# Kernel tuning notes

Hardware: AMD Instinct MI355X
Metric: run time of the kernel (lower is better)

The kernel has to match this reference:

```python
import jax, jax.numpy as jnp
import numpy as np

HEADS = 6
EPS = 1e-5


def _na_idx(L, k, d):
    # NATTEN-style dilated neighborhood: work within dilation cosets,
    # clamp window to stay inside the image (window shifts at borders).
    i = np.arange(L)
    g = i % d
    p = i // d
    Lg = (L - g + d - 1) // d  # coset length per position
    start = np.clip(p - k // 2, 0, Lg - k)
    j = np.arange(k)
    nbr = g[:, None] + d * (start[:, None] + j[None, :])          # [L,k] neighbor coords
    rel = (start[:, None] + j[None, :]) - p[:, None] + (k - 1)    # [L,k] rpb index in [0,2k-2]
    return jnp.asarray(nbr, jnp.int32), jnp.asarray(rel, jnp.int32)


def _na2d(x, qkv_w, qkv_b, proj_w, proj_b, rpb, heads, k, d):
    # x: [B,H,W,C] NHWC neighborhood attention with relative positional bias
    B, H, W, C = x.shape
    dh = C // heads
    scale = dh ** -0.5
    qkv = (x @ qkv_w + qkv_b).reshape(B, H, W, 3, heads, dh)
    qkv = jnp.transpose(qkv, (3, 0, 4, 1, 2, 5))  # [3,B,h,H,W,dh]
    q, kk, v = qkv[0] * scale, qkv[1], qkv[2]
    nh, rh = _na_idx(H, k, d)
    nw, rw = _na_idx(W, k, d)

    def gather(t):  # [B,h,H,W,dh] -> [B,h,H,W,k,k,dh]
        t = t[:, :, nh]              # [B,h,H,k,W,dh]
        t = t[:, :, :, :, nw]        # [B,h,H,k,W,k,dh]
        return jnp.transpose(t, (0, 1, 2, 4, 3, 5, 6))

    kn, vn = gather(kk), gather(v)
    attn = jnp.einsum('bhxyd,bhxyijd->bhxyij', q, kn)  # [B,h,H,W,k,k]
    bias = rpb[:, rh]                  # [h,H,k,2k-1]
    bias = bias[:, :, :, rw]           # [h,H,k,W,k]
    bias = jnp.transpose(bias, (0, 1, 3, 2, 4))  # [h,H,W,k,k]
    attn = attn + bias[None]
    attn = jax.nn.softmax(attn.reshape(B, heads, H, W, k * k), axis=-1)
    attn = attn.reshape(B, heads, H, W, k, k)
    out = jnp.einsum('bhxyij,bhxyijd->bhxyd', attn, vn)
    out = jnp.transpose(out, (0, 2, 3, 1, 4)).reshape(B, H, W, C)
    return out @ proj_w + proj_b


def _rln(x, w, b, m1_w, m1_b, m2_w, m2_b):
    # Revised LayerNorm: normalize over (C,H,W) per sample; meta1/meta2 are 1x1 convs on std/mean
    mean = jnp.mean(x, axis=(1, 2, 3), keepdims=True)
    std = jnp.sqrt(jnp.mean((x - mean) ** 2, axis=(1, 2, 3), keepdims=True) + EPS)
    out = (x - mean) / std * w + b
    rescale = m1_w[None, :, None, None] * std + m1_b[None, :, None, None]
    rebias = m2_w[None, :, None, None] * mean + m2_b[None, :, None, None]
    return out, rescale, rebias


def _c11(x, w, b):  # 1x1 conv on NCHW == per-pixel linear
    return jnp.einsum('bchw,oc->bohw', x, w) + b[None, :, None, None]


def _gelu(x):
    return jax.nn.gelu(x, approximate=False)


def reference(x, ln_w, ln_b, m1_w, m1_b, m2_w, m2_b, qkv1_w, qkv1_b, proj1_w, proj1_b, rpb1, qkv2_w, qkv2_b, proj2_w, proj2_b, rpb2, mlp_w1, mlp_b1, mlp_w2, mlp_b2, bn_g, bn_b, bn_m, bn_v, pa_w1, pa_b1, pa_w2, pa_b2, ca_w1, ca_b1, ca_w2, ca_b2, m2a_w1, m2a_b1, m2a_w2, m2a_b2):
    # ---- NA block 1 (kernel 7, dilation 1) ----
    sc = x
    y, rs, rb = _rln(x, ln_w, ln_b, m1_w, m1_b, m2_w, m2_b)
    a = _na2d(jnp.transpose(y, (0, 2, 3, 1)), qkv1_w, qkv1_b, proj1_w, proj1_b, rpb1, HEADS, 7, 1)
    x = sc + jnp.transpose(a, (0, 3, 1, 2)) * rs + rb
    # ---- NA block 2 (kernel 5, dilation 8) ----
    sc = x
    y, rs, rb = _rln(x, ln_w, ln_b, m1_w, m1_b, m2_w, m2_b)
    a = _na2d(jnp.transpose(y, (0, 2, 3, 1)), qkv2_w, qkv2_b, proj2_w, proj2_b, rpb2, HEADS, 5, 8)
    x = sc + jnp.transpose(a, (0, 3, 1, 2)) * rs + rb
    # ---- MLP (source reuses the pre-attn2 shortcut `sc`) ----
    y, rs, rb = _rln(x, ln_w, ln_b, m1_w, m1_b, m2_w, m2_b)
    m = _c11(jax.nn.relu(_c11(y, mlp_w1, mlp_b1)), mlp_w2, mlp_b2)
    x = sc + m * rs + rb
    # ---- BN + pixel attention + channel attention + mlp2 ----
    sc = x
    inv = jax.lax.rsqrt(bn_v + EPS)
    y = (x - bn_m[None, :, None, None]) * (inv * bn_g)[None, :, None, None] + bn_b[None, :, None, None]
    pa = jax.nn.sigmoid(_c11(_gelu(_c11(y, pa_w1, pa_b1)), pa_w2, pa_b2))  # [B,1,H,W]
    y = pa * y
    gap = jnp.mean(y, axis=(2, 3), keepdims=True)
    ca = jax.nn.sigmoid(_c11(_gelu(_c11(gap, ca_w1, ca_b1)), ca_w2, ca_b2))  # [B,C,1,1]
    y = ca * y
    y = _c11(_gelu(_c11(y, m2a_w1, m2a_b1)), m2a_w2, m2a_b2)
    return sc + y


def setup_inputs() -> dict:
    key = jax.random.key(0)
    B, C, H, W, HID = 4, 96, 64, 64, 384
    ks = iter(jax.random.split(key, 48))

    def rn(shape, s=0.02):
        return jax.random.normal(next(ks), shape, jnp.float32) * s

    d = {}
    d['x'] = jax.random.normal(next(ks), (B, C, H, W), jnp.float32)
    d['ln_w'] = jnp.ones((1, C, 1, 1), jnp.float32)
    d['ln_b'] = jnp.zeros((1, C, 1, 1), jnp.float32)
    d['m1_w'] = rn((C,)); d['m1_b'] = jnp.ones((C,), jnp.float32)
    d['m2_w'] = rn((C,)); d['m2_b'] = jnp.zeros((C,), jnp.float32)
    d['qkv1_w'] = rn((C, 3 * C)); d['qkv1_b'] = jnp.zeros((3 * C,), jnp.float32)
    d['proj1_w'] = rn((C, C)); d['proj1_b'] = jnp.zeros((C,), jnp.float32)
    d['rpb1'] = rn((HEADS, 13, 13))
    d['qkv2_w'] = rn((C, 3 * C)); d['qkv2_b'] = jnp.zeros((3 * C,), jnp.float32)
    d['proj2_w'] = rn((C, C)); d['proj2_b'] = jnp.zeros((C,), jnp.float32)
    d['rpb2'] = rn((HEADS, 9, 9))
    d['mlp_w1'] = rn((HID, C)); d['mlp_b1'] = jnp.zeros((HID,), jnp.float32)
    d['mlp_w2'] = rn((C, HID)); d['mlp_b2'] = jnp.zeros((C,), jnp.float32)
    d['bn_g'] = jnp.ones((C,), jnp.float32); d['bn_b'] = jnp.zeros((C,), jnp.float32)
    d['bn_m'] = jnp.zeros((C,), jnp.float32); d['bn_v'] = jnp.ones((C,), jnp.float32)
    d['pa_w1'] = rn((C // 8, C)); d['pa_b1'] = jnp.zeros((C // 8,), jnp.float32)
    d['pa_w2'] = rn((1, C // 8)); d['pa_b2'] = jnp.zeros((1,), jnp.float32)
    d['ca_w1'] = rn((C, C)); d['ca_b1'] = jnp.zeros((C,), jnp.float32)
    d['ca_w2'] = rn((C, C)); d['ca_b2'] = jnp.zeros((C,), jnp.float32)
    d['m2a_w1'] = rn((C, C)); d['m2a_b1'] = jnp.zeros((C,), jnp.float32)
    d['m2a_w2'] = rn((C, C)); d['m2a_b2'] = jnp.zeros((C,), jnp.float32)
    return d
```

## Files before the change

kernel.cpp:

```cpp
#include <hip/hip_runtime.h>
#include <math.h>

#define CC 96
#define NP 4096
#define NHEADS 6
#define NELEMF 393216.0f
#define EPSF 1e-5f

typedef __attribute__((ext_vector_type(8))) short bf16x8;
typedef __attribute__((ext_vector_type(4))) float f32x4;
#define MFMA16(a,b,c) __builtin_amdgcn_mfma_f32_16x16x32_bf16(a,b,c,0,0,0)

#define WQKV1  64
#define WQKV2  (WQKV1+13824)
#define WPROJ1 (WQKV2+13824)
#define WPROJ2 (WPROJ1+4608)
#define WMLP1  (WPROJ2+4608)
#define WMLP2  (WMLP1+18432)
#define WM2A1  (WMLP2+18432)
#define WM2A2  (WM2A1+4608)
#define WPA1T  (WM2A2+4608)
#define WBNS   (WPA1T+1152)
#define WCA1T  (WBNS+192)
#define WCA2T  (WCA1T+9216)
#define WS_Q   870784
#define WS_K   (WS_Q+786432)
#define WS_V   (WS_K+786432)
#define WS_ATTPM (WS_V+786432)
#define WS_X1  (WS_ATTPM+786432)
#define WS_X2  (WS_X1+1572864)
#define WS_X3  (WS_X2+1572864)
#define WS_PA  (WS_X3+1572864)
#define WS_GAP (WS_PA+16384)

__device__ __forceinline__ float gelu_f(float x){
  return 0.5f * x * (1.0f + erff(x * 0.7071067811865476f));
}
__device__ __forceinline__ float sigmoid_f(float x){
  return 1.0f / (1.0f + __expf(-x));
}
__device__ __forceinline__ unsigned short bfr(float f){
  unsigned int u = __float_as_uint(f);
  u += 0x7fffu + ((u >> 16) & 1u);
  return (unsigned short)(u >> 16);
}
__device__ __forceinline__ float bflo16(unsigned short u){ return __uint_as_float(((unsigned int)u) << 16); }
__device__ __forceinline__ float bflo(unsigned int u){ return __uint_as_float(u << 16); }
__device__ __forceinline__ float bfhi(unsigned int u){ return __uint_as_float(u & 0xffff0000u); }
__device__ __forceinline__ void get_ms(const float* st, int b, float& mean, float& inv, float& stdv){
  float s = st[b], s2 = st[4+b];
  mean = s * (1.0f/NELEMF);
  float var = fmaxf(s2 * (1.0f/NELEMF) - mean*mean, 0.0f);
  stdv = sqrtf(var + EPSF);
  inv = 1.0f / stdv;
}
__device__ __forceinline__ float ldf(const float* p, int i){ return p[i]; }
__device__ __forceinline__ float ldf(const unsigned short* p, int i){ return bflo16(p[i]); }
__device__ __forceinline__ void load4(const float* p, float4& v){ v = *(const float4*)p; }
__device__ __forceinline__ void load4(const unsigned short* p, float4& v){
  ushort4 u = *(const ushort4*)p;
  v.x = bflo16(u.x); v.y = bflo16(u.y); v.z = bflo16(u.z); v.w = bflo16(u.w);
}

__device__ __forceinline__ float dot16(const float* qv, const uint2* col, int ww){
  uint2 a0 = col[ww], a1 = col[64+ww], a2 = col[128+ww], a3 = col[192+ww];
  float s;
  s  = qv[0]*bflo(a0.x);           s = fmaf(qv[1],  bfhi(a0.x), s);
  s = fmaf(qv[2],  bflo(a0.y), s); s = fmaf(qv[3],  bfhi(a0.y), s);
  s = fmaf(qv[4],  bflo(a1.x), s); s = fmaf(qv[5],  bfhi(a1.x), s);
  s = fmaf(qv[6],  bflo(a1.y), s); s = fmaf(qv[7],  bfhi(a1.y), s);
  s = fmaf(qv[8],  bflo(a2.x), s); s = fmaf(qv[9],  bfhi(a2.x), s);
  s = fmaf(qv[10], bflo(a2.y), s); s = fmaf(qv[11], bfhi(a2.y), s);
  s = fmaf(qv[12], bflo(a3.x), s); s = fmaf(qv[13], bfhi(a3.x), s);
  s = fmaf(qv[14], bflo(a3.y), s); s = fmaf(qv[15], bfhi(a3.y), s);
  return s;
}
__device__ __forceinline__ void pv16(float w, const uint2* col, int ww, float* acc){
  uint2 a0 = col[ww], a1 = col[64+ww], a2 = col[128+ww], a3 = col[192+ww];
  acc[0]  = fmaf(w, bflo(a0.x), acc[0]);  acc[1]  = fmaf(w, bfhi(a0.x), acc[1]);
  acc[2]  = fmaf(w, bflo(a0.y), acc[2]);  acc[3]  = fmaf(w, bfhi(a0.y), acc[3]);
  acc[4]  = fmaf(w, bflo(a1.x), acc[4]);  acc[5]  = fmaf(w, bfhi(a1.x), acc[5]);
  acc[6]  = fmaf(w, bflo(a1.y), acc[6]);  acc[7]  = fmaf(w, bfhi(a1.y), acc[7]);
  acc[8]  = fmaf(w, bflo(a2.x), acc[8]);  acc[9]  = fmaf(w, bfhi(a2.x), acc[9]);
  acc[10] = fmaf(w, bflo(a2.y), acc[10]); acc[11] = fmaf(w, bfhi(a2.y), acc[11]);
  acc[12] = fmaf(w, bflo(a3.x), acc[12]); acc[13] = fmaf(w, bfhi(a3.x), acc[13]);
  acc[14] = fmaf(w, bflo(a3.y), acc[14]); acc[15] = fmaf(w, bfhi(a3.y), acc[15]);
}

__global__ void prep_stats_kernel(const float* __restrict__ x, float* __restrict__ st,
                             const float* __restrict__ q1, const float* __restrict__ q2,
                             const float* __restrict__ p1, const float* __restrict__ p2,
                             const float* __restrict__ w1, const float* __restrict__ w2,
                             const float* __restrict__ a1, const float* __restrict__ a2,
                             const float* __restrict__ pw1,
                             const float* __restrict__ bg, const float* __restrict__ bb,
                             const float* __restrict__ bm, const float* __restrict__ bv,
                             const float* __restrict__ cw1, const float* __restrict__ cw2,
                             float* __restrict__ ws){
  if(blockIdx.x < 384){
    int b = blockIdx.x / CC, c = blockIdx.x % CC;
    const float4* p4 = (const float4*)(x + (size_t)(b*CC + c)*NP);
    float s = 0.f, s2 = 0.f;
    for(int i = threadIdx.x; i < 1024; i += 256){
      float4 v = p4[i];
      s += v.x + v.y + v.z + v.w;
      s2 = fmaf(v.x, v.x, fmaf(v.y, v.y, fmaf(v.z, v.z, fmaf(v.w, v.w, s2))));
    }
    for(int off = 32; off > 0; off >>= 1){ s += __shfl_down(s, off); s2 += __shfl_down(s2, off); }
    __shared__ float ls[8];
    int wid = threadIdx.x >> 6;
    if((threadIdx.x & 63) == 0){ ls[wid] = s; ls[4+wid] = s2; }
    __syncthreads();
    if(threadIdx.x == 0){
      atomicAdd(&st[b],   ls[0]+ls[1]+ls[2]+ls[3]);
      atomicAdd(&st[4+b], ls[4]+ls[5]+ls[6]+ls[7]);
    }
    return;
  }
  int gid = (blockIdx.x - 384)*256 + threadIdx.x;
  if(gid < 27648){ int n = gid/96, c = gid%96; ((unsigned short*)(ws+WQKV1))[gid] = bfr(q1[c*288+n]); }
  else if(gid < 55296){ int g = gid-27648; int n = g/96, c = g%96; ((unsigned short*)(ws+WQKV2))[g] = bfr(q2[c*288+n]); }
  else if(gid < 64512){ int g = gid-55296; int n = g/96, c = g%96; ((unsigned short*)(ws+WPROJ1))[g] = bfr(p1[c*96+n]); }
  else if(gid < 73728){ int g = gid-64512; int n = g/96, c = g%96; ((unsigned short*)(ws+WPROJ2))[g] = bfr(p2[c*96+n]); }
  else if(gid < 110592){ int g = gid-73728; ((unsigned short*)(ws+WMLP1))[g] = bfr(w1[g]); }
  else if(gid < 147456){ int g = gid-110592; ((unsigned short*)(ws+WMLP2))[g] = bfr(w2[g]); }
  else if(gid < 156672){ int g = gid-147456; ((unsigned short*)(ws+WM2A1))[g] = bfr(a1[g]); }
  else if(gid < 165888){ int g = gid-156672; ((unsigned short*)(ws+WM2A2))[g] = bfr(a2[g]); }
  else if(gid < 167040){ int g = gid-165888; int c = g/12, h = g%12; ws[WPA1T + g] = pw1[h*96+c]; }
  else if(gid < 167136){ int c = gid-167040;
    float sc = rsqrtf(bv[c] + EPSF) * bg[c];
    ws[WBNS + c] = sc;
    ws[WBNS + 96 + c] = bb[c] - bm[c]*sc;
  }
  else if(gid < 167520){ ws[WS_GAP + (gid-167136)] = 0.f; }
  else if(gid < 176736){ int g = gid-167520; int o = g/96, c = g%96; ws[WCA1T + c*96 + o] = cw1[g]; }
  else if(gid < 185952){ int g = gid-176736; int o = g/96, c = g%96; ws[WCA2T + c*96 + o] = cw2[g]; }
}

template<typename AT>
__global__ void __launch_bounds__(512) gemm_qkv_kernel(
    const AT* __restrict__ xin, const float* __restrict__ st,
    const float* __restrict__ lnw, const float* __restrict__ lnb,
    const unsigned short* __restrict__ wT, const float* __restrict__ qb,
    unsigned short* __restrict__ qo, unsigned short* __restrict__ ko, unsigned short* __restrict__ vo){
  __shared__ unsigned short Atl[64*104];
  __shared__ float scl[96], ofs[96];
  int m_base = blockIdx.x*64;
  int b = m_base >> 12, pxl0 = m_base & 4095;
  float mean, inv, stdv; get_ms(st, b, mean, inv, stdv);
  int tid = threadIdx.x;
  if(tid < 96){ float s = inv*lnw[tid]; scl[tid] = s; ofs[tid] = lnb[tid] - mean*s; }
  __syncthreads();
  const AT* src = xin + (size_t)b*CC*NP + pxl0;
  for(int idx = tid; idx < 96*16; idx += 512){
    int c = idx >> 4, p4 = (idx & 15) << 2;
    float4 v; load4(src + (size_t)c*NP + p4, v);
    float s = scl[c], o = ofs[c];
    Atl[(p4+0)*104 + c] = bfr(fmaf(v.x, s, o));
    Atl[(p4+1)*104 + c] = bfr(fmaf(v.y, s, o));
    Atl[(p4+2)*104 + c] = bfr(fmaf(v.z, s, o));
    Atl[(p4+3)*104 + c] = bfr(fmaf(v.w, s, o));
  }
  __syncthreads();
  int w = tid >> 6, lane = tid & 63, ml = lane & 15, q = lane >> 4;
  int row = w & 3, nh = w >> 2;
  const unsigned short* arow = Atl + (row*16 + ml)*104;
  bf16x8 av[3];
  #pragma unroll
  for(int ks = 0; ks < 3; ++ks) av[ks] = *(const bf16x8*)(arow + ks*32 + q*8);
  f32x4 z = {0.f,0.f,0.f,0.f};
  #pragma unroll
  for(int g0 = 0; g0 < 3; ++g0){
    int g = nh*3 + g0;
    f32x4 acc[3] = {z, z, z};
    #pragma unroll
    for(int ks = 0; ks < 3; ++ks){
      #pragma unroll
      for(int gg = 0; gg < 3; ++gg){
        bf16x8 bv = *(const bf16x8*)(wT + (g*48 + gg*16 + ml)*96 + ks*32 + q*8);
        acc[gg] = MFMA16(av[ks], bv, acc[gg]);
      }
    }
    #pragma unroll
    for(int gg = 0; gg < 3; ++gg){
      int nfb = g*48 + gg*16;
      int t = nfb/96, head = (nfb%96) >> 4;
      float scale = (t == 0) ? 0.25f : 1.0f;
      unsigned short* dst = (t == 0) ? qo : (t == 1) ? ko : vo;
      float bias = qb[nfb + ml];
      #pragma unroll
      for(int r = 0; r < 4; ++r){
        int pxl = pxl0 + row*16 + q*4 + r;
        dst[(((size_t)(b*NHEADS + head))*NP + pxl)*16 + ml] = bfr((acc[gg][r] + bias)*scale);
      }
    }
  }
}

template<typename SCT>
__global__ void __launch_bounds__(512) gemm_proj_kernel(
    const unsigned short* __restrict__ attpm, const unsigned short* __restrict__ wT,
    const float* __restrict__ pb, const SCT* __restrict__ scx, const float* __restrict__ st,
    const float* __restrict__ m1w, const float* __restrict__ m1b,
    const float* __restrict__ m2w, const float* __restrict__ m2b,
    unsigned short* __restrict__ dst, float* __restrict__ st_out){
  int w = threadIdx.x >> 6, lane = threadIdx.x & 63;
  int ml = lane & 15, q = lane >> 4;
  int m_base = blockIdx.x*128 + w*16;
  int n0 = blockIdx.y*48;
  f32x4 z = {0.f,0.f,0.f,0.f};
  f32x4 acc[3] = {z, z, z};
  {
    const bf16x8* a0 = (const bf16x8*)(attpm + (size_t)(m_base + ml)*96 + q*8);
    #pragma unroll
    for(int ks = 0; ks < 3; ++ks){
      bf16x8 av0 = a0[ks*4];
      #pragma unroll
      for(int g = 0; g < 3; ++g){
        bf16x8 bv = *(const bf16x8*)(wT + (n0 + g*16 + ml)*96 + ks*32 + q*8);
        acc[g] = MFMA16(av0, bv, acc[g]);
      }
    }
  }
  __shared__ float T[48*133];
  #pragma unroll
  for(int g = 0; g < 3; ++g)
    #pragma unroll
    for(int r = 0; r < 4; ++r)
      T[(g*16 + ml)*133 + w*16 + q*4 + r] = acc[g][r];
  __syncthreads();
  int b = (blockIdx.x*128) >> 12, pxl0 = (blockIdx.x*128) & 4095;
  float mean, inv, stdv; get_ms(st, b, mean, inv, stdv);
  float s = 0.f, s2 = 0.f;
  for(int idx = threadIdx.x; idx < 48*128; idx += 512){
    int row = idx >> 7, px = idx & 127;
    int n = n0 + row;
    float rsf = fmaf(m1w[n], stdv, m1b[n]);
    float rbf = fmaf(m2w[n], mean, m2b[n]);
    int ad = (b*CC + n)*NP + pxl0 + px;
    float val = ldf(scx, ad) + (T[row*133 + px] + pb[n])*rsf + rbf;
    dst[ad] = bfr(val);
    s += val; s2 = fmaf(val, val, s2);
  }
  for(int off = 32; off > 0; off >>= 1){ s += __shfl_down(s, off); s2 += __shfl_down(s2, off); }
  __shared__ float ls[16];
  int wid = threadIdx.x >> 6;
  if((threadIdx.x & 63) == 0){ ls[wid] = s; ls[8+wid] = s2; }
  __syncthreads();
  if(threadIdx.x == 0){
    atomicAdd(&st_out[b],   ls[0]+ls[1]+ls[2]+ls[3]+ls[4]+ls[5]+ls[6]+ls[7]);
    atomicAdd(&st_out[4+b], ls[8]+ls[9]+ls[10]+ls[11]+ls[12]+ls[13]+ls[14]+ls[15]);
  }
}

__global__ void __launch_bounds__(512) gemm_mlp_kernel(
    const unsigned short* __restrict__ xin, const float* __restrict__ st,
    const float* __restrict__ lnw, const float* __restrict__ lnb,
    const unsigned short* __restrict__ w1T, const float* __restrict__ b1,
    const unsigned short* __restrict__ w2T, const float* __restrict__ b2,
    const unsigned short* __restrict__ scx,
    const float* __restrict__ m1w, const float* __restrict__ m1b,
    const float* __restrict__ m2w, const float* __restrict__ m2b,
    float* __restrict__ dst,
    const float* __restrict__ bns, const float* __restrict__ pw1t,
    const float* __restrict__ pb1, const float* __restrict__ pw2,
    const float* __restrict__ pb2, float* __restrict__ pa,
    float* __restrict__ gap){
  __shared__ __align__(16) char smbuf[63488];
  __shared__ float scl[96], ofs[96];
  unsigned short* Atl  = (unsigned short*)smbuf;
  unsigned short* hidL = (unsigned short*)(smbuf + 13312);
  float* T = (float*)(smbuf + 13312);
  float* gpart = (float*)smbuf;
  int m_base = blockIdx.x*64;
  int b = m_base >> 12, pxl0 = m_base & 4095;
  float mean, inv, stdv; get_ms(st, b, mean, inv, stdv);
  int tid = threadIdx.x;
  if(tid < 96){ float s = inv*lnw[tid]; scl[tid] = s; ofs[tid] = lnb[tid] - mean*s; }
  __syncthreads();
  const unsigned short* src = xin + (size_t)b*CC*NP + pxl0;
  for(int idx = tid; idx < 96*16; idx += 512){
    int c = idx >> 4, p4 = (idx & 15) << 2;
    float4 v; load4(src + (size_t)c*NP + p4, v);
    float s = scl[c], o = ofs[c];
    Atl[(p4+0)*104 + c] = bfr(fmaf(v.x, s, o));
    Atl[(p4+1)*104 + c] = bfr(fmaf(v.y, s, o));
    Atl[(p4+2)*104 + c] = bfr(fmaf(v.z, s, o));
    Atl[(p4+3)*104 + c] = bfr(fmaf(v.w, s, o));
  }
  __syncthreads();
  int w = tid >> 6, lane = tid & 63, ml = lane & 15, q = lane >> 4;
  int row = w & 3, nh = w >> 2;
  f32x4 z = {0.f,0.f,0.f,0.f};
  {
    const unsigned short* arow = Atl + (row*16 + ml)*104;
    bf16x8 av[3];
    #pragma unroll
    for(int ks = 0; ks < 3; ++ks) av[ks] = *(const bf16x8*)(arow + ks*32 + q*8);
    #pragma unroll
    for(int g0 = 0; g0 < 4; ++g0){
      int g = nh*4 + g0;
      f32x4 acc[3] = {z, z, z};
      #pragma unroll
      for(int ks = 0; ks < 3; ++ks){
        #pragma unroll
        for(int gg = 0; gg < 3; ++gg){
          bf16x8 bv = *(const bf16x8*)(w1T + (g*48 + gg*16 + ml)*96 + ks*32 + q*8);
          acc[gg] = MFMA16(av[ks], bv, acc[gg]);
        }
      }
      #pragma unroll
      for(int gg = 0; gg < 3; ++gg){
        int n = g*48 + gg*16 + ml;
        float bias = b1[n];
        #pragma unroll
        for(int r = 0; r < 4; ++r)
          hidL[(row*16 + q*4 + r)*392 + n] = bfr(fmaxf(acc[gg][r] + bias, 0.f));
      }
    }
  }
  __syncthreads();
  f32x4 acc2[3] = {z, z, z};
  {
    const unsigned short* arow = hidL + (row*16 + ml)*392;
    #pragma unroll
    for(int ks = 0; ks < 12; ++ks){
      bf16x8 av = *(const bf16x8*)(arow + ks*32 + q*8);
      #pragma unroll
      for(int g0 = 0; g0 < 3; ++g0){
        int g = nh*3 + g0;
        bf16x8 bv = *(const bf16x8*)(w2T + (g*16 + ml)*384 + ks*32 + q*8);
        acc2[g0] = MFMA16(av, bv, acc2[g0]);
      }
    }
  }
  __syncthreads();
  #pragma unroll
  for(int g0 = 0; g0 < 3; ++g0){
    int g = nh*3 + g0;
    #pragma unroll
    for(int r = 0; r < 4; ++r)
      T[(g*16 + ml)*68 + row*16 + q*4 + r] = acc2[g0][r];
  }
  __syncthreads();
  for(int idx = tid; idx < 96*64; idx += 512){
    int n = idx >> 6, px = idx & 63;
    float rsf = fmaf(m1w[n], stdv, m1b[n]);
    float rbf = fmaf(m2w[n], mean, m2b[n]);
    int ad = (b*CC + n)*NP + pxl0 + px;
    float val = ldf(scx, ad) + (T[n*68 + px] + b2[n])*rsf + rbf;
    dst[ad] = val;
    T[n*68 + px] = val;
  }
  __syncthreads();
  int pxq = tid >> 3, t = tid & 7;
  float yvv[12], acc[12];
  #pragma unroll
  for(int h = 0; h < 12; ++h) acc[h] = 0.f;
  #pragma unroll 6
  for(int cc = 0; cc < 12; ++cc){
    int c = t*12 + cc;
    float yv = fmaf(T[c*68 + pxq], bns[c], bns[96 + c]);
    yvv[cc] = yv;
    #pragma unroll
    for(int h = 0; h < 12; ++h) acc[h] = fmaf(yv, pw1t[c*12 + h], acc[h]);
  }
  #pragma unroll
  for(int h = 0; h < 12; ++h){
    acc[h] += __shfl_xor(acc[h], 1);
    acc[h] += __shfl_xor(acc[h], 2);
    acc[h] += __shfl_xor(acc[h], 4);
  }
  float s = pb2[0];
  #pragma unroll
  for(int h = 0; h < 12; ++h) s = fmaf(gelu_f(acc[h] + pb1[h]), pw2[h], s);
  float pav = sigmoid_f(s);
  if(t == 0) pa[b*NP + pxl0 + pxq] = pav;
  #pragma unroll 6
  for(int cc = 0; cc < 12; ++cc){
    float g = yvv[cc] * pav;
    g += __shfl_xor(g, 8);  g += __shfl_xor(g, 16); g += __shfl_xor(g, 32);
    if(lane < 8) gpart[w*96 + lane*12 + cc] = g;
  }
  __syncthreads();
  if(tid < 96){
    int c = tid;
    float v = 0.f;
    #pragma unroll
    for(int ww = 0; ww < 8; ++ww) v += gpart[ww*96 + c];
    atomicAdd(&gap[b*96 + c], v * (1.0f/4096.0f));
  }
}

__global__ void __launch_bounds__(512) gemm_m2a_kernel(
    const float* __restrict__ x3, const float* __restrict__ bns,
    const float* __restrict__ pa, const float* __restrict__ gap,
    const float* __restrict__ cw1T, const float* __restrict__ cb1,
    const float* __restrict__ cw2T, const float* __restrict__ cb2,
    const unsigned short* __restrict__ w1T, const float* __restrict__ b1,
    const unsigned short* __restrict__ w2T, const float* __restrict__ b2,
    const float* __restrict__ scx, float* __restrict__ outp){
  __shared__ __align__(16) char smbuf[26624];
  __shared__ float scl[96], ofs[96], pal[64];
  __shared__ float gl[96], tl[96];
  unsigned short* Atl = (unsigned short*)smbuf;
  unsigned short* tl2 = (unsigned short*)(smbuf + 13312);
  float* T = (float*)smbuf;
  int m_base = blockIdx.x*64;
  int b = m_base >> 12, pxl0 = m_base & 4095;
  int tid = threadIdx.x;
  if(tid < 96) gl[tid] = gap[b*96 + tid];
  if(tid >= 128 && tid < 192) pal[tid-128] = pa[m_base + (tid-128)];
  __syncthreads();
  if(tid < 96){
    float a = cb1[tid];
    #pragma unroll 8
    for(int c = 0; c < 96; ++c) a = fmaf(gl[c], cw1T[c*96 + tid], a);
    tl[tid] = gelu_f(a);
  }
  __syncthreads();
  if(tid < 96){
    float a = cb2[tid];
    #pragma unroll 8
    for(int c = 0; c < 96; ++c) a = fmaf(tl[c], cw2T[c*96 + tid], a);
    float cv = sigmoid_f(a);
    scl[tid] = bns[tid]*cv; ofs[tid] = bns[96+tid]*cv;
  }
  __syncthreads();
  const float* src = x3 + (size_t)b*CC*NP + pxl0;
  for(int idx = tid; idx < 96*16; idx += 512){
    int c = idx >> 4, p4 = (idx & 15) << 2;
    float4 v = *(const float4*)(src + (size_t)c*NP + p4);
    float s = scl[c], o = ofs[c];
    Atl[(p4+0)*104 + c] = bfr(fmaf(v.x, s, o) * pal[p4+0]);
    Atl[(p4+1)*104 + c] = bfr(fmaf(v.y, s, o) * pal[p4+1]);
    Atl[(p4+2)*104 + c] = bfr(fmaf(v.z, s, o) * pal[p4+2]);
    Atl[(p4+3)*104 + c] = bfr(fmaf(v.w, s, o) * pal[p4+3]);
  }
  __syncthreads();
  int w = tid >> 6, lane = tid & 63, ml = lane & 15, q = lane >> 4;
  int row = w & 3, nh = w >> 2;
  f32x4 z = {0.f,0.f,0.f,0.f};
  f32x4 acc1[3] = {z, z, z};
  {
    const unsigned short* arow = Atl + (row*16 + ml)*104;
    #pragma unroll
    for(int ks = 0; ks < 3; ++ks){
      bf16x8 av = *(const bf16x8*)(arow + ks*32 + q*8);
      #pragma unroll
      for(int g0 = 0; g0 < 3; ++g0){
        int g = nh*3 + g0;
        bf16x8 bv = *(const bf16x8*)(w1T + (g*16 + ml)*96 + ks*32 + q*8);
        acc1[g0] = MFMA16(av, bv, acc1[g0]);
      }
    }
  }
  #pragma unroll
  for(int g0 = 0; g0 < 3; ++g0){
    int g = nh*3 + g0;
    float bias = b1[g*16 + ml];
    #pragma unroll
    for(int r = 0; r < 4; ++r)
      tl2[(row*16 + q*4 + r)*104 + g*16 + ml] = bfr(gelu_f(acc1[g0][r] + bias));
  }
  __syncthreads();
  f32x4 acc2[3] = {z, z, z};
  {
    const unsigned short* arow = tl2 + (row*16 + ml)*104;
    #pragma unroll
    for(int ks = 0; ks < 3; ++ks){
      bf16x8 av = *(const bf16x8*)(arow + ks*32 + q*8);
      #pragma unroll
      for(int g0 = 0; g0 < 3; ++g0){
        int g = nh*3 + g0;
        bf16x8 bv = *(const bf16x8*)(w2T + (g*16 + ml)*96 + ks*32 + q*8);
        acc2[g0] = MFMA16(av, bv, acc2[g0]);
      }
    }
  }
  __syncthreads();
  #pragma unroll
  for(int g0 = 0; g0 < 3; ++g0){
    int g = nh*3 + g0;
    #pragma unroll
    for(int r = 0; r < 4; ++r)
      T[(g*16 + ml)*68 + row*16 + q*4 + r] = acc2[g0][r];
  }
  __syncthreads();
  for(int idx = tid; idx < 96*64; idx += 512){
    int n = idx >> 6, p = idx & 63;
    int ad = (b*CC + n)*NP + pxl0 + p;
    outp[ad] = scx[ad] + T[n*68 + p] + b2[n];
  }
}

template<int K, int D, int RPB, int SPAN>
__global__ void __launch_bounds__(256) attn2_kernel(
    const unsigned short* __restrict__ qb, const unsigned short* __restrict__ kb,
    const unsigned short* __restrict__ vb, const float* __restrict__ rpb,
    unsigned short* __restrict__ outp){
  __shared__ uint2 kst[SPAN*256];
  __shared__ uint2 vst[SPAN*256];
  __shared__ float rpbl[RPB*RPB];
  int bh = blockIdx.x >> 4;
  int quad = blockIdx.x & 15;
  int head = bh % NHEADS, b = bh / NHEADS;
  int tid = threadIdx.x;
  int tcol = tid >> 6, y = tid & 63;

  int gx, px, px0;
  if(D == 1){ gx = 0; px = quad*4 + tcol; px0 = quad*4; }
  else      { gx = quad & (D-1); px = (quad >> 3)*4 + tcol; px0 = (quad >> 3)*4; }
  int Lgx = (64 - gx + D - 1) / D;
  int sx = min(max(px - K/2, 0), Lgx - K);
  int sxmin = min(max(px0 - K/2, 0), Lgx - K);
  int nstage = min(SPAN, Lgx - sxmin);

  for(int i = tid; i < RPB*RPB; i += 256) rpbl[i] = rpb[head*RPB*RPB + i];
  {
    const uint2* kg = (const uint2*)(kb + (size_t)bh*NP*16);
    const uint2* vg = (const uint2*)(vb + (size_t)bh*NP*16);
    int spx = tid & 63, sq = tid >> 6;
    for(int c = 0; c < nstage; ++c){
      int hh = gx + D*(sxmin + c);
      kst[c*256 + sq*64 + spx] = kg[hh*256 + spx*4 + sq];
      vst[c*256 + sq*64 + spx] = vg[hh*256 + spx*4 + sq];
    }
  }
  int x = gx + D*px;
  int pix = x*64 + y;
  float qv[16];
  {
    const uint4* qg = (const uint4*)(qb + ((size_t)bh*NP + pix)*16);
    uint4 qa = qg[0], qb4 = qg[1];
    qv[0]=bflo(qa.x);  qv[1]=bfhi(qa.x);  qv[2]=bflo(qa.y);  qv[3]=bfhi(qa.y);
    qv[4]=bflo(qa.z);  qv[5]=bfhi(qa.z);  qv[6]=bflo(qa.w);  qv[7]=bfhi(qa.w);
    qv[8]=bflo(qb4.x); qv[9]=bfhi(qb4.x); qv[10]=bflo(qb4.y);qv[11]=bfhi(qb4.y);
    qv[12]=bflo(qb4.z);qv[13]=bfhi(qb4.z);qv[14]=bflo(qb4.w);qv[15]=bfhi(qb4.w);
  }
  __syncthreads();

  int gy = y & (D-1), py = (D==1) ? y : (y >> 3);
  int Lgy = (64 - gy + D - 1) / D;
  int sy = min(max(py - K/2, 0), Lgy - K);
  int dxb = sx - px + (K-1);
  int dyb = sy - py + (K-1);
  int ci0 = sx - sxmin;

  float sc[K*K];
  #pragma unroll
  for(int i = 0; i < K; ++i){
    const uint2* kc = kst + (ci0 + i)*256;
    const float* br = rpbl + (i + dxb)*RPB + dyb;
    #pragma unroll
    for(int j = 0; j < K; ++j){
      int ww = gy + D*(sy + j);
      sc[i*K + j] = dot16(qv, kc, ww) + br[j];
    }
  }
  float mx = -1e30f;
  #pragma unroll
  for(int n = 0; n < K*K; ++n) mx = fmaxf(mx, sc[n]);
  float sum = 0.f;
  #pragma unroll
  for(int n = 0; n < K*K; ++n){ float e = __expf(sc[n] - mx); sc[n] = e; sum += e; }
  float rs = 1.0f / sum;
  float acc[16];
  #pragma unroll
  for(int d = 0; d < 16; ++d) acc[d] = 0.f;
  #pragma unroll
  for(int i = 0; i < K; ++i){
    const uint2* vc = vst + (ci0 + i)*256;
    #pragma unroll
    for(int j = 0; j < K; ++j){
      int ww = gy + D*(sy + j);
      pv16(sc[i*K + j] * rs, vc, ww, acc);
    }
  }
  unsigned int ow[8];
  #pragma unroll
  for(int p = 0; p < 8; ++p)
    ow[p] = (unsigned int)bfr(acc[2*p]) | ((unsigned int)bfr(acc[2*p+1]) << 16);
  unsigned short* op = outp + ((size_t)(b*NP + pix))*96 + head*16;
  ((uint4*)op)[0] = make_uint4(ow[0], ow[1], ow[2], ow[3]);
  ((uint4*)op)[1] = make_uint4(ow[4], ow[5], ow[6], ow[7]);
}

extern "C" void kernel_launch(void* const* d_in, const int* in_sizes, int n_in,
                              void* d_out, int out_size, void* d_ws, size_t ws_size,
                              hipStream_t stream){
  (void)in_sizes; (void)n_in; (void)out_size; (void)ws_size;
  const float* x     = (const float*)d_in[0];
  const float* lnw   = (const float*)d_in[1];
  const float* lnb   = (const float*)d_in[2];
  const float* m1w   = (const float*)d_in[3];
  const float* m1b   = (const float*)d_in[4];
  const float* m2w   = (const float*)d_in[5];
  const float* m2b   = (const float*)d_in[6];
  const float* qkv1w = (const float*)d_in[7];
  const float* qkv1b = (const float*)d_in[8];
  const float* proj1w= (const float*)d_in[9];
  const float* proj1b= (const float*)d_in[10];
  const float* rpb1  = (const float*)d_in[11];
  const float* qkv2w = (const float*)d_in[12];
  const float* qkv2b = (const float*)d_in[13];
  const float* proj2w= (const float*)d_in[14];
  const float* proj2b= (const float*)d_in[15];
  const float* rpb2  = (const float*)d_in[16];
  const float* mw1   = (const float*)d_in[17];
  const float* mb1   = (const float*)d_in[18];
  const float* mw2   = (const float*)d_in[19];
  const float* mb2   = (const float*)d_in[20];
  const float* bng   = (const float*)d_in[21];
  const float* bnb   = (const float*)d_in[22];
  const float* bnm   = (const float*)d_in[23];
  const float* bnv   = (const float*)d_in[24];
  const float* paw1  = (const float*)d_in[25];
  const float* pab1  = (const float*)d_in[26];
  const float* paw2  = (const float*)d_in[27];
  const float* pab2  = (const float*)d_in[28];
  const float* caw1  = (const float*)d_in[29];
  const float* cab1  = (const float*)d_in[30];
  const float* caw2  = (const float*)d_in[31];
  const float* cab2  = (const float*)d_in[32];
  const float* aw1   = (const float*)d_in[33];
  const float* ab1   = (const float*)d_in[34];
  const float* aw2   = (const float*)d_in[35];
  const float* ab2   = (const float*)d_in[36];

  float* ws  = (float*)d_ws;
  float* out = (float*)d_out;
  float* st0 = ws;
  float* st1 = ws + 8;
  float* st2 = ws + 16;
  unsigned short* q     = (unsigned short*)(ws + WS_Q);
  unsigned short* k     = (unsigned short*)(ws + WS_K);
  unsigned short* v     = (unsigned short*)(ws + WS_V);
  unsigned short* attpm = (unsigned short*)(ws + WS_ATTPM);
  unsigned short* x1b   = (unsigned short*)(ws + WS_X1);
  unsigned short* x2b   = (unsigned short*)(ws + WS_X2);
  float* x3  = ws + WS_X3;
  float* pab = ws + WS_PA;
  float* gpb = ws + WS_GAP;
  float* bns = ws + WBNS;

  hipMemsetAsync(d_ws, 0, 64*sizeof(float), stream);
  prep_stats_kernel<<<1111, 256, 0, stream>>>(x, st0, qkv1w, qkv2w, proj1w, proj2w,
                                              mw1, mw2, aw1, aw2, paw1,
                                              bng, bnb, bnm, bnv, caw1, caw2, ws);

  gemm_qkv_kernel<float><<<256, 512, 0, stream>>>(x, st0, lnw, lnb,
      (unsigned short*)(ws+WQKV1), qkv1b, q, k, v);
  attn2_kernel<7,1,13,10><<<384, 256, 0, stream>>>(q, k, v, rpb1, attpm);
  gemm_proj_kernel<float><<<dim3(128,2), 512, 0, stream>>>(attpm, (unsigned short*)(ws+WPROJ1),
      proj1b, x, st0, m1w, m1b, m2w, m2b, x1b, st1);

  gemm_qkv_kernel<unsigned short><<<256, 512, 0, stream>>>(x1b, st1, lnw, lnb,
      (unsigned short*)(ws+WQKV2), qkv2b, q, k, v);
  attn2_kernel<5,8,9,6><<<384, 256, 0, stream>>>(q, k, v, rpb2, attpm);
  gemm_proj_kernel<unsigned short><<<dim3(128,2), 512, 0, stream>>>(attpm, (unsigned short*)(ws+WPROJ2),
      proj2b, x1b, st1, m1w, m1b, m2w, m2b, x2b, st2);

  gemm_mlp_kernel<<<256, 512, 0, stream>>>(x2b, st2, lnw, lnb,
      (unsigned short*)(ws+WMLP1), mb1, (unsigned short*)(ws+WMLP2), mb2,
      x1b, m1w, m1b, m2w, m2b, x3,
      bns, ws + WPA1T, pab1, paw2, pab2, pab, gpb);

  gemm_m2a_kernel<<<256, 512, 0, stream>>>(x3, bns, pab, gpb,
                                           ws + WCA1T, cab1, ws + WCA2T, cab2,
                                           (unsigned short*)(ws+WM2A1), ab1,
                                           (unsigned short*)(ws+WM2A2), ab2, x3, out);
}
```

Baseline: 263.6 us.

## Fuse neighborhood attention with output projection and drop LDS K/V staging

```diff
diff --git a/kernel.cpp b/kernel.cpp
--- a/kernel.cpp
+++ b/kernel.cpp
@@ -62,29 +62,29 @@
   v.x = bflo16(u.x); v.y = bflo16(u.y); v.z = bflo16(u.z); v.w = bflo16(u.w);
 }
 
-__device__ __forceinline__ float dot16(const float* qv, const uint2* col, int ww){
-  uint2 a0 = col[ww], a1 = col[64+ww], a2 = col[128+ww], a3 = col[192+ww];
+__device__ __forceinline__ float dotg(const float* qv, const uint4* p){
+  uint4 a = p[0], b = p[1];
   float s;
-  s  = qv[0]*bflo(a0.x);           s = fmaf(qv[1],  bfhi(a0.x), s);
-  s = fmaf(qv[2],  bflo(a0.y), s); s = fmaf(qv[3],  bfhi(a0.y), s);
-  s = fmaf(qv[4],  bflo(a1.x), s); s = fmaf(qv[5],  bfhi(a1.x), s);
-  s = fmaf(qv[6],  bflo(a1.y), s); s = fmaf(qv[7],  bfhi(a1.y), s);
-  s = fmaf(qv[8],  bflo(a2.x), s); s = fmaf(qv[9],  bfhi(a2.x), s);
-  s = fmaf(qv[10], bflo(a2.y), s); s = fmaf(qv[11], bfhi(a2.y), s);
-  s = fmaf(qv[12], bflo(a3.x), s); s = fmaf(qv[13], bfhi(a3.x), s);
-  s = fmaf(qv[14], bflo(a3.y), s); s = fmaf(qv[15], bfhi(a3.y), s);
+  s  = qv[0]*bflo(a.x);            s = fmaf(qv[1],  bfhi(a.x), s);
+  s = fmaf(qv[2],  bflo(a.y), s);  s = fmaf(qv[3],  bfhi(a.y), s);
+  s = fmaf(qv[4],  bflo(a.z), s);  s = fmaf(qv[5],  bfhi(a.z), s);
+  s = fmaf(qv[6],  bflo(a.w), s);  s = fmaf(qv[7],  bfhi(a.w), s);
+  s = fmaf(qv[8],  bflo(b.x), s);  s = fmaf(qv[9],  bfhi(b.x), s);
+  s = fmaf(qv[10], bflo(b.y), s);  s = fmaf(qv[11], bfhi(b.y), s);
+  s = fmaf(qv[12], bflo(b.z), s);  s = fmaf(qv[13], bfhi(b.z), s);
+  s = fmaf(qv[14], bflo(b.w), s);  s = fmaf(qv[15], bfhi(b.w), s);
   return s;
 }
-__device__ __forceinline__ void pv16(float w, const uint2* col, int ww, float* acc){
-  uint2 a0 = col[ww], a1 = col[64+ww], a2 = col[128+ww], a3 = col[192+ww];
-  acc[0]  = fmaf(w, bflo(a0.x), acc[0]);  acc[1]  = fmaf(w, bfhi(a0.x), acc[1]);
-  acc[2]  = fmaf(w, bflo(a0.y), acc[2]);  acc[3]  = fmaf(w, bfhi(a0.y), acc[3]);
-  acc[4]  = fmaf(w, bflo(a1.x), acc[4]);  acc[5]  = fmaf(w, bfhi(a1.x), acc[5]);
-  acc[6]  = fmaf(w, bflo(a1.y), acc[6]);  acc[7]  = fmaf(w, bfhi(a1.y), acc[7]);
-  acc[8]  = fmaf(w, bflo(a2.x), acc[8]);  acc[9]  = fmaf(w, bfhi(a2.x), acc[9]);
-  acc[10] = fmaf(w, bflo(a2.y), acc[10]); acc[11] = fmaf(w, bfhi(a2.y), acc[11]);
-  acc[12] = fmaf(w, bflo(a3.x), acc[12]); acc[13] = fmaf(w, bfhi(a3.x), acc[13]);
-  acc[14] = fmaf(w, bflo(a3.y), acc[14]); acc[15] = fmaf(w, bfhi(a3.y), acc[15]);
+__device__ __forceinline__ void pvg(float w, const uint4* p, float* acc){
+  uint4 a = p[0], b = p[1];
+  acc[0]  = fmaf(w, bflo(a.x), acc[0]);  acc[1]  = fmaf(w, bfhi(a.x), acc[1]);
+  acc[2]  = fmaf(w, bflo(a.y), acc[2]);  acc[3]  = fmaf(w, bfhi(a.y), acc[3]);
+  acc[4]  = fmaf(w, bflo(a.z), acc[4]);  acc[5]  = fmaf(w, bfhi(a.z), acc[5]);
+  acc[6]  = fmaf(w, bflo(a.w), acc[6]);  acc[7]  = fmaf(w, bfhi(a.w), acc[7]);
+  acc[8]  = fmaf(w, bflo(b.x), acc[8]);  acc[9]  = fmaf(w, bfhi(b.x), acc[9]);
+  acc[10] = fmaf(w, bflo(b.y), acc[10]); acc[11] = fmaf(w, bfhi(b.y), acc[11]);
+  acc[12] = fmaf(w, bflo(b.z), acc[12]); acc[13] = fmaf(w, bfhi(b.z), acc[13]);
+  acc[14] = fmaf(w, bflo(b.w), acc[14]); acc[15] = fmaf(w, bfhi(b.w), acc[15]);
 }
 
 __global__ void prep_stats_kernel(const float* __restrict__ x, float* __restrict__ st,
@@ -197,59 +197,143 @@
   }
 }
 
-template<typename SCT>
-__global__ void __launch_bounds__(512) gemm_proj_kernel(
-    const unsigned short* __restrict__ attpm, const unsigned short* __restrict__ wT,
-    const float* __restrict__ pb, const SCT* __restrict__ scx, const float* __restrict__ st,
+template<int K, int D, int RPB, typename SCT>
+__global__ void __launch_bounds__(512) attnproj_kernel(
+    const unsigned short* __restrict__ qb, const unsigned short* __restrict__ kb,
+    const unsigned short* __restrict__ vb, const float* __restrict__ rpb,
+    const unsigned short* __restrict__ wT, const float* __restrict__ pb,
+    const SCT* __restrict__ scx, const float* __restrict__ st,
     const float* __restrict__ m1w, const float* __restrict__ m1b,
     const float* __restrict__ m2w, const float* __restrict__ m2b,
     unsigned short* __restrict__ dst, float* __restrict__ st_out){
-  int w = threadIdx.x >> 6, lane = threadIdx.x & 63;
-  int ml = lane & 15, q = lane >> 4;
-  int m_base = blockIdx.x*128 + w*16;
-  int n0 = blockIdx.y*48;
+  __shared__ __align__(16) char smbuf[26624];
+  __shared__ float rpbl[NHEADS*RPB*RPB];
+  __shared__ float ls[16];
+  unsigned short* attout = (unsigned short*)smbuf;
+  float* T = (float*)smbuf;
+  int b = blockIdx.x >> 6;
+  int x = blockIdx.x & 63;
+  int tid = threadIdx.x;
+  for(int i = tid; i < NHEADS*RPB*RPB; i += 512) rpbl[i] = rpb[i];
+  __syncthreads();
+
+  if(tid < 384){
+    int head = tid >> 6;
+    int y = tid & 63;
+    int bh = b*NHEADS + head;
+    int gx = (D == 1) ? 0 : (x & (D-1));
+    int px = (D == 1) ? x : (x >> 3);
+    int Lgx = (64 - gx + D - 1) / D;
+    int sx = min(max(px - K/2, 0), Lgx - K);
+    int gy = (D == 1) ? 0 : (y & (D-1));
+    int py = (D == 1) ? y : (y >> 3);
+    int Lgy = (64 - gy + D - 1) / D;
+    int sy = min(max(py - K/2, 0), Lgy - K);
+    int dxb = sx - px + (K-1);
+    int dyb = sy - py + (K-1);
+    int pix = x*64 + y;
+
+    float qv[16];
+    {
+      const uint4* qg = (const uint4*)(qb + ((size_t)bh*NP + pix)*16);
+      uint4 qa = qg[0], qb4 = qg[1];
+      qv[0]=bflo(qa.x);  qv[1]=bfhi(qa.x);  qv[2]=bflo(qa.y);  qv[3]=bfhi(qa.y);
+      qv[4]=bflo(qa.z);  qv[5]=bfhi(qa.z);  qv[6]=bflo(qa.w);  qv[7]=bfhi(qa.w);
+      qv[8]=bflo(qb4.x); qv[9]=bfhi(qb4.x); qv[10]=bflo(qb4.y);qv[11]=bfhi(qb4.y);
+      qv[12]=bflo(qb4.z);qv[13]=bfhi(qb4.z);qv[14]=bflo(qb4.w);qv[15]=bfhi(qb4.w);
+    }
+    const unsigned short* kgb = kb + (size_t)bh*NP*16;
+    const unsigned short* vgb = vb + (size_t)bh*NP*16;
+
+    float sc[K*K];
+    #pragma unroll
+    for(int i = 0; i < K; ++i){
+      int colx = gx + D*(sx + i);
+      const unsigned short* kcol = kgb + (size_t)colx*64*16;
+      const float* br = rpbl + (head*RPB + (i + dxb))*RPB + dyb;
+      #pragma unroll
+      for(int j = 0; j < K; ++j){
+        int wwy = gy + D*(sy + j);
+        sc[i*K + j] = dotg(qv, (const uint4*)(kcol + wwy*16)) + br[j];
+      }
+    }
+    float mx = -1e30f;
+    #pragma unroll
+    for(int n = 0; n < K*K; ++n) mx = fmaxf(mx, sc[n]);
+    float sum = 0.f;
+    #pragma unroll
+    for(int n = 0; n < K*K; ++n){ float e = __expf(sc[n] - mx); sc[n] = e; sum += e; }
+    float rs = 1.0f / sum;
+    float acc[16];
+    #pragma unroll
+    for(int d = 0; d < 16; ++d) acc[d] = 0.f;
+    #pragma unroll
+    for(int i = 0; i < K; ++i){
+      int colx = gx + D*(sx + i);
+      const unsigned short* vcol = vgb + (size_t)colx*64*16;
+      #pragma unroll
+      for(int j = 0; j < K; ++j){
+        int wwy = gy + D*(sy + j);
+        pvg(sc[i*K + j] * rs, (const uint4*)(vcol + wwy*16), acc);
+      }
+    }
+    unsigned int ow[8];
+    #pragma unroll
+    for(int p = 0; p < 8; ++p)
+      ow[p] = (unsigned int)bfr(acc[2*p]) | ((unsigned int)bfr(acc[2*p+1]) << 16);
+    unsigned short* op = attout + y*104 + head*16;
+    *(uint4*)op = make_uint4(ow[0], ow[1], ow[2], ow[3]);
+    *(uint4*)(op + 8) = make_uint4(ow[4], ow[5], ow[6], ow[7]);
+  }
+  __syncthreads();
+
+  int w = tid >> 6, lane = tid & 63, ml = lane & 15, q = lane >> 4;
+  int row = w & 3, nh = w >> 2;
   f32x4 z = {0.f,0.f,0.f,0.f};
   f32x4 acc[3] = {z, z, z};
   {
-    const bf16x8* a0 = (const bf16x8*)(attpm + (size_t)(m_base + ml)*96 + q*8);
+    const unsigned short* arow = attout + (row*16 + ml)*104;
     #pragma unroll
     for(int ks = 0; ks < 3; ++ks){
-      bf16x8 av0 = a0[ks*4];
-      #pragma unroll
-      for(int g = 0; g < 3; ++g){
-        bf16x8 bv = *(const bf16x8*)(wT + (n0 + g*16 + ml)*96 + ks*32 + q*8);
-        acc[g] = MFMA16(av0, bv, acc[g]);
-      }
-    }
-  }
-  __shared__ float T[48*133];
-  #pragma unroll
-  for(int g = 0; g < 3; ++g)
+      bf16x8 av = *(const bf16x8*)(arow + ks*32 + q*8);
+      #pragma unroll
+      for(int g0 = 0; g0 < 3; ++g0){
+        int g = nh*3 + g0;
+        bf16x8 bv = *(const bf16x8*)(wT + (g*16 + ml)*96 + ks*32 + q*8);
+        acc[g0] = MFMA16(av, bv, acc[g0]);
+      }
+    }
+  }
+  __syncthreads();
+  #pragma unroll
+  for(int g0 = 0; g0 < 3; ++g0){
+    int g = nh*3 + g0;
     #pragma unroll
     for(int r = 0; r < 4; ++r)
-      T[(g*16 + ml)*133 + w*16 + q*4 + r] = acc[g][r];
-  __syncthreads();
-  int b = (blockIdx.x*128) >> 12, pxl0 = (blockIdx.x*128) & 4095;
+      T[(g*16 + ml)*68 + row*16 + q*4 + r] = acc[g0][r];
+  }
+  __syncthreads();
+  int pxl0 = x*64;
   float mean, inv, stdv; get_ms(st, b, mean, inv, stdv);
   float s = 0.f, s2 = 0.f;
-  for(int idx = threadIdx.x; idx < 48*128; idx += 512){
-    int row = idx >> 7, px = idx & 127;
-    int n = n0 + row;
+  for(int idx = tid; idx < 96*64; idx += 512){
+    int n = idx >> 6, p = idx & 63;
     float rsf = fmaf(m1w[n], stdv, m1b[n]);
     float rbf = fmaf(m2w[n], mean, m2b[n]);
-    int ad = (b*CC + n)*NP + pxl0 + px;
-    float val = ldf(scx, ad) + (T[row*133 + px] + pb[n])*rsf + rbf;
+    int ad = (b*CC + n)*NP + pxl0 + p;
+    float val = ldf(scx, ad) + (T[n*68 + p] + pb[n])*rsf + rbf;
     dst[ad] = bfr(val);
     s += val; s2 = fmaf(val, val, s2);
   }
   for(int off = 32; off > 0; off >>= 1){ s += __shfl_down(s, off); s2 += __shfl_down(s2, off); }
-  __shared__ float ls[16];
-  int wid = threadIdx.x >> 6;
-  if((threadIdx.x & 63) == 0){ ls[wid] = s; ls[8+wid] = s2; }
-  __syncthreads();
-  if(threadIdx.x == 0){
-    atomicAdd(&st_out[b],   ls[0]+ls[1]+ls[2]+ls[3]+ls[4]+ls[5]+ls[6]+ls[7]);
-    atomicAdd(&st_out[4+b], ls[8]+ls[9]+ls[10]+ls[11]+ls[12]+ls[13]+ls[14]+ls[15]);
+  if(lane == 0){ ls[w] = s; ls[8+w] = s2; }
+  __syncthreads();
+  if(tid == 0){
+    float a0 = 0.f, a1 = 0.f;
+    #pragma unroll
+    for(int i = 0; i < 8; ++i){ a0 += ls[i]; a1 += ls[8+i]; }
+    atomicAdd(&st_out[b], a0);
+    atomicAdd(&st_out[4+b], a1);
   }
 }
 
@@ -492,98 +576,6 @@
     int ad = (b*CC + n)*NP + pxl0 + p;
     outp[ad] = scx[ad] + T[n*68 + p] + b2[n];
   }
-}
-
-template<int K, int D, int RPB, int SPAN>
-__global__ void __launch_bounds__(256) attn2_kernel(
-    const unsigned short* __restrict__ qb, const unsigned short* __restrict__ kb,
-    const unsigned short* __restrict__ vb, const float* __restrict__ rpb,
-    unsigned short* __restrict__ outp){
-  __shared__ uint2 kst[SPAN*256];
-  __shared__ uint2 vst[SPAN*256];
-  __shared__ float rpbl[RPB*RPB];
-  int bh = blockIdx.x >> 4;
-  int quad = blockIdx.x & 15;
-  int head = bh % NHEADS, b = bh / NHEADS;
-  int tid = threadIdx.x;
-  int tcol = tid >> 6, y = tid & 63;
-
-  int gx, px, px0;
-  if(D == 1){ gx = 0; px = quad*4 + tcol; px0 = quad*4; }
-  else      { gx = quad & (D-1); px = (quad >> 3)*4 + tcol; px0 = (quad >> 3)*4; }
-  int Lgx = (64 - gx + D - 1) / D;
-  int sx = min(max(px - K/2, 0), Lgx - K);
-  int sxmin = min(max(px0 - K/2, 0), Lgx - K);
-  int nstage = min(SPAN, Lgx - sxmin);
-
-  for(int i = tid; i < RPB*RPB; i += 256) rpbl[i] = rpb[head*RPB*RPB + i];
-  {
-    const uint2* kg = (const uint2*)(kb + (size_t)bh*NP*16);
-    const uint2* vg = (const uint2*)(vb + (size_t)bh*NP*16);
-    int spx = tid & 63, sq = tid >> 6;
-    for(int c = 0; c < nstage; ++c){
-      int hh = gx + D*(sxmin + c);
-      kst[c*256 + sq*64 + spx] = kg[hh*256 + spx*4 + sq];
-      vst[c*256 + sq*64 + spx] = vg[hh*256 + spx*4 + sq];
-    }
-  }
-  int x = gx + D*px;
-  int pix = x*64 + y;
-  float qv[16];
-  {
-    const uint4* qg = (const uint4*)(qb + ((size_t)bh*NP + pix)*16);
-    uint4 qa = qg[0], qb4 = qg[1];
-    qv[0]=bflo(qa.x);  qv[1]=bfhi(qa.x);  qv[2]=bflo(qa.y);  qv[3]=bfhi(qa.y);
-    qv[4]=bflo(qa.z);  qv[5]=bfhi(qa.z);  qv[6]=bflo(qa.w);  qv[7]=bfhi(qa.w);
-    qv[8]=bflo(qb4.x); qv[9]=bfhi(qb4.x); qv[10]=bflo(qb4.y);qv[11]=bfhi(qb4.y);
-    qv[12]=bflo(qb4.z);qv[13]=bfhi(qb4.z);qv[14]=bflo(qb4.w);qv[15]=bfhi(qb4.w);
-  }
-  __syncthreads();
-
-  int gy = y & (D-1), py = (D==1) ? y : (y >> 3);
-  int Lgy = (64 - gy + D - 1) / D;
-  int sy = min(max(py - K/2, 0), Lgy - K);
-  int dxb = sx - px + (K-1);
-  int dyb = sy - py + (K-1);
-  int ci0 = sx - sxmin;
-
-  float sc[K*K];
-  #pragma unroll
-  for(int i = 0; i < K; ++i){
-    const uint2* kc = kst + (ci0 + i)*256;
-    const float* br = rpbl + (i + dxb)*RPB + dyb;
-    #pragma unroll
-    for(int j = 0; j < K; ++j){
-      int ww = gy + D*(sy + j);
-      sc[i*K + j] = dot16(qv, kc, ww) + br[j];
-    }
-  }
-  float mx = -1e30f;
-  #pragma unroll
-  for(int n = 0; n < K*K; ++n) mx = fmaxf(mx, sc[n]);
-  float sum = 0.f;
-  #pragma unroll
-  for(int n = 0; n < K*K; ++n){ float e = __expf(sc[n] - mx); sc[n] = e; sum += e; }
-  float rs = 1.0f / sum;
-  float acc[16];
-  #pragma unroll
-  for(int d = 0; d < 16; ++d) acc[d] = 0.f;
-  #pragma unroll
-  for(int i = 0; i < K; ++i){
-    const uint2* vc = vst + (ci0 + i)*256;
-    #pragma unroll
-    for(int j = 0; j < K; ++j){
-      int ww = gy + D*(sy + j);
-      pv16(sc[i*K + j] * rs, vc, ww, acc);
-    }
-  }
-  unsigned int ow[8];
-  #pragma unroll
-  for(int p = 0; p < 8; ++p)
-    ow[p] = (unsigned int)bfr(acc[2*p]) | ((unsigned int)bfr(acc[2*p+1]) << 16);
-  unsigned short* op = outp + ((size_t)(b*NP + pix))*96 + head*16;
-  ((uint4*)op)[0] = make_uint4(ow[0], ow[1], ow[2], ow[3]);
-  ((uint4*)op)[1] = make_uint4(ow[4], ow[5], ow[6], ow[7]);
 }
 
 extern "C" void kernel_launch(void* const* d_in, const int* in_sizes, int n_in,
@@ -636,7 +628,6 @@
   unsigned short* q     = (unsigned short*)(ws + WS_Q);
   unsigned short* k     = (unsigned short*)(ws + WS_K);
   unsigned short* v     = (unsigned short*)(ws + WS_V);
-  unsigned short* attpm = (unsigned short*)(ws + WS_ATTPM);
   unsigned short* x1b   = (unsigned short*)(ws + WS_X1);
   unsigned short* x2b   = (unsigned short*)(ws + WS_X2);
   float* x3  = ws + WS_X3;
@@ -651,15 +642,13 @@
 
   gemm_qkv_kernel<float><<<256, 512, 0, stream>>>(x, st0, lnw, lnb,
       (unsigned short*)(ws+WQKV1), qkv1b, q, k, v);
-  attn2_kernel<7,1,13,10><<<384, 256, 0, stream>>>(q, k, v, rpb1, attpm);
-  gemm_proj_kernel<float><<<dim3(128,2), 512, 0, stream>>>(attpm, (unsigned short*)(ws+WPROJ1),
-      proj1b, x, st0, m1w, m1b, m2w, m2b, x1b, st1);
+  attnproj_kernel<7,1,13,float><<<256, 512, 0, stream>>>(q, k, v, rpb1,
+      (unsigned short*)(ws+WPROJ1), proj1b, x, st0, m1w, m1b, m2w, m2b, x1b, st1);
 
   gemm_qkv_kernel<unsigned short><<<256, 512, 0, stream>>>(x1b, st1, lnw, lnb,
       (unsigned short*)(ws+WQKV2), qkv2b, q, k, v);
-  attn2_kernel<5,8,9,6><<<384, 256, 0, stream>>>(q, k, v, rpb2, attpm);
-  gemm_proj_kernel<unsigned short><<<dim3(128,2), 512, 0, stream>>>(attpm, (unsigned short*)(ws+WPROJ2),
-      proj2b, x1b, st1, m1w, m1b, m2w, m2b, x2b, st2);
+  attnproj_kernel<5,8,9,unsigned short><<<256, 512, 0, stream>>>(q, k, v, rpb2,
+      (unsigned short*)(ws+WPROJ2), proj2b, x1b, st1, m1w, m1b, m2w, m2b, x2b, st2);
 
   gemm_mlp_kernel<<<256, 512, 0, stream>>>(x2b, st2, lnw, lnb,
       (unsigned short*)(ws+WMLP1), mb1, (unsigned short*)(ws+WMLP2), mb2,
```

Result: faster. 251.0 us (-4.8%).
